# Optimization experiments

Measured on AMD Instinct MI355X. Metric: run time of the kernel, lower is better.

## Reference

```python
import jax, jax.numpy as jnp
import numpy as np

N = 50000      # nodes
E = 800000     # edges
D_IN, D_H, D_OUT = 256, 256, 128
BN_EPS = 1e-5


def setup_inputs() -> dict:
    key = jax.random.key(0)
    ks = jax.random.split(key, 16)
    inp = {}
    inp["x"] = jax.random.normal(ks[0], (N, D_IN), dtype=jnp.float32)
    inp["edge_index"] = jax.random.randint(ks[1], (2, E), 0, N, dtype=jnp.int32)
    s1 = 1.0 / np.sqrt(D_IN)
    s2 = 1.0 / np.sqrt(D_H)
    inp["W1"] = jax.random.normal(ks[2], (D_IN, D_H), dtype=jnp.float32) * s1
    inp["b1"] = jnp.zeros((D_H,), dtype=jnp.float32)
    inp["g1"] = jnp.ones((D_H,), dtype=jnp.float32)
    inp["be1"] = jnp.zeros((D_H,), dtype=jnp.float32)
    inp["m1"] = jax.random.normal(ks[3], (D_H,), dtype=jnp.float32) * 0.1
    inp["v1"] = jax.random.uniform(ks[4], (D_H,), dtype=jnp.float32, minval=0.5, maxval=1.5)
    inp["W2"] = jax.random.normal(ks[5], (D_H, D_H), dtype=jnp.float32) * s2
    inp["b2"] = jnp.zeros((D_H,), dtype=jnp.float32)
    inp["g2"] = jnp.ones((D_H,), dtype=jnp.float32)
    inp["be2"] = jnp.zeros((D_H,), dtype=jnp.float32)
    inp["m2"] = jax.random.normal(ks[6], (D_H,), dtype=jnp.float32) * 0.1
    inp["v2"] = jax.random.uniform(ks[7], (D_H,), dtype=jnp.float32, minval=0.5, maxval=1.5)
    inp["W3"] = jax.random.normal(ks[8], (D_H, D_OUT), dtype=jnp.float32) * s2
    inp["b3"] = jnp.zeros((D_OUT,), dtype=jnp.float32)
    return inp


def reference(x, edge_index, W1, b1, g1, be1, m1, v1,
              W2, b2, g2, be2, m2, v2, W3, b3):
    # Add self-loops (PyG GCNConv default) and compute symmetric normalization once.
    loop = jnp.arange(N, dtype=edge_index.dtype)
    src = jnp.concatenate([edge_index[0], loop])   # [E+N]
    dst = jnp.concatenate([edge_index[1], loop])   # [E+N]
    deg = jax.ops.segment_sum(jnp.ones_like(dst, dtype=x.dtype), dst, num_segments=N)
    dinv = jax.lax.rsqrt(deg)                      # deg >= 1 thanks to self-loops
    norm = (dinv[src] * dinv[dst])[:, None]        # [E+N, 1]

    def gcn_conv(h, W, b):
        h = h @ W                                   # [N, D]
        agg = jax.ops.segment_sum(h[src] * norm, dst, num_segments=N)
        return agg + b

    def bn_eval(h, g, be, m, v):
        return (h - m) * (g * jax.lax.rsqrt(v + BN_EPS)) + be

    h = jax.nn.relu(bn_eval(gcn_conv(x, W1, b1), g1, be1, m1, v1))  # dropout = identity (eval)
    h = jax.nn.relu(bn_eval(gcn_conv(h, W2, b2), g2, be2, m2, v2))
    out = gcn_conv(h, W3, b3)                       # [N, D_OUT]
    return out
```

## Files before the change

### kernel.cpp

```cpp
#include <hip/hip_runtime.h>
#include <hip/hip_bf16.h>
#include <hip/hip_fp16.h>


#define GN 50000
#define GE 800000

typedef float f32x4 __attribute__((ext_vector_type(4)));
typedef _Float16 f16x8 __attribute__((ext_vector_type(8)));


__global__ __launch_bounds__(256) void init_kernel(int* counts, int* cursor, int* total) {
    int i = blockIdx.x * 256 + threadIdx.x;
    if (i < GN) { counts[i] = 0; cursor[i] = 0; }
    if (i == 0) *total = 0;
}

__global__ __launch_bounds__(256) void count_kernel(const int* __restrict__ dst, int* __restrict__ counts) {
    int e = blockIdx.x * 256 + threadIdx.x;
    if (e < GE) atomicAdd(&counts[dst[e]], 1);
}

__global__ __launch_bounds__(256) void alloc_kernel(const int* __restrict__ counts, float* __restrict__ dinv,
                                                    int* __restrict__ base, int* __restrict__ total) {
    int i = blockIdx.x * 256 + threadIdx.x;
    int lane = threadIdx.x & 63;
    int c = (i < GN) ? counts[i] : 0;
    if (i < GN) dinv[i] = rsqrtf((float)c + 1.0f);
    int v = c;
#pragma unroll
    for (int off = 1; off < 64; off <<= 1) {
        int t = __shfl_up(v, off);
        if (lane >= off) v += t;
    }
    int waveSum = __shfl(v, 63);
    int wb = 0;
    if (lane == 63) wb = atomicAdd(total, waveSum);
    wb = __shfl(wb, 63);
    if (i < GN) base[i] = wb + v - c;
}

__global__ __launch_bounds__(256) void fill_kernel(const int* __restrict__ src, const int* __restrict__ dst,
                                                   const int* __restrict__ base, int* __restrict__ cursor,
                                                   int* __restrict__ col) {
    int e = blockIdx.x * 256 + threadIdx.x;
    if (e < GE) {
        int d = dst[e];
        int pos = base[d] + atomicAdd(&cursor[d], 1);
        col[pos] = src[e];
    }
}

__global__ __launch_bounds__(256) void params_kernel(
    const float* b1, const float* g1, const float* be1, const float* m1, const float* v1,
    const float* b2, const float* g2, const float* be2, const float* m2, const float* v2,
    float* prm) {
    int t = threadIdx.x;
    float s1 = g1[t] * rsqrtf(v1[t] + 1e-5f);
    prm[0 * 256 + t] = s1;
    prm[1 * 256 + t] = (b1[t] - m1[t]) * s1 + be1[t];
    float s2 = g2[t] * rsqrtf(v2[t] + 1e-5f);
    prm[2 * 256 + t] = s2;
    prm[3 * 256 + t] = (b2[t] - m2[t]) * s2 + be2[t];
}


__global__ __launch_bounds__(256) void conv_x(const float* __restrict__ in, ushort* __restrict__ out, int n4) {
    int i = blockIdx.x * 256 + threadIdx.x;
    if (i >= n4) return;
    float4 v = *(const float4*)&in[(size_t)i * 4];
    ushort4 h;
    h.x = __half_as_ushort(__float2half_rn(v.x));
    h.y = __half_as_ushort(__float2half_rn(v.y));
    h.z = __half_as_ushort(__float2half_rn(v.z));
    h.w = __half_as_ushort(__float2half_rn(v.w));
    *(ushort4*)&out[(size_t)i * 4] = h;
}

__global__ __launch_bounds__(256) void transpose_all(const float* __restrict__ W1, const float* __restrict__ W2,
                                                     const float* __restrict__ W3,
                                                     ushort* __restrict__ T1h, ushort* __restrict__ T1l,
                                                     ushort* __restrict__ T2h, ushort* __restrict__ T2l,
                                                     ushort* __restrict__ T3h, ushort* __restrict__ T3l) {
    int idx = blockIdx.x * 256 + threadIdx.x;
    const float* W;
    ushort *Th, *Tl;
    int i, DO;
    if (idx < 65536) { W = W1; Th = T1h; Tl = T1l; i = idx; DO = 256; }
    else if (idx < 131072) { W = W2; Th = T2h; Tl = T2l; i = idx - 65536; DO = 256; }
    else if (idx < 163840) { W = W3; Th = T3h; Tl = T3l; i = idx - 131072; DO = 128; }
    else return;
    int n = i >> 8, k = i & 255;
    float v = W[k * DO + n];
    __half h = __float2half_rn(v);
    Th[i] = __half_as_ushort(h);
    Tl[i] = __half_as_ushort(__float2half_rn(v - __half2float(h)));
}


template <int DO>
__global__ __launch_bounds__(256) void gemm_mfma(const ushort* __restrict__ A16, const ushort* __restrict__ Bhi,
                                                 const ushort* __restrict__ Blo, const float* __restrict__ dinv,
                                                 __half* __restrict__ C, int M) {
    __shared__ ushort lds[3][128][40];
    int tid = threadIdx.x;
    int lane = tid & 63;
    int wave = tid >> 6;
    int wm = wave >> 1, wn = wave & 1;
    int m0 = blockIdx.x * 128;
    int n0 = blockIdx.y * 128;
    int rsel = lane & 15;
    int ksel = (lane >> 4) * 8;

    f32x4 acc[4][4] = {};

    for (int k0 = 0; k0 < 256; k0 += 32) {
        auto stage = [&](const ushort* __restrict__ src, int baseRow, int rClamp, int p) {
#pragma unroll
            for (int j = 0; j < 2; j++) {
                int o = (tid + j * 256) * 16;
                int row = o >> 6;
                int kb = o & 63;
                int rg = min(baseRow + row, rClamp);
                uint4 v = *(const uint4*)((const char*)src + (size_t)rg * 512 + (size_t)k0 * 2 + kb);
                *(uint4*)((char*)&lds[p][row][0] + kb) = v;
            }
        };
        stage(A16, m0, M - 1, 0);
        stage(Bhi, n0, DO - 1, 1);
        stage(Blo, n0, DO - 1, 2);
        __syncthreads();

        f16x8 bh[4], bl[4];
#pragma unroll
        for (int ni = 0; ni < 4; ni++) {
            bh[ni] = *(const f16x8*)&lds[1][wn * 64 + ni * 16 + rsel][ksel];
            bl[ni] = *(const f16x8*)&lds[2][wn * 64 + ni * 16 + rsel][ksel];
        }
#pragma unroll
        for (int mi = 0; mi < 4; mi++) {
            f16x8 av = *(const f16x8*)&lds[0][wm * 64 + mi * 16 + rsel][ksel];
#pragma unroll
            for (int ni = 0; ni < 4; ni++) {
                acc[mi][ni] = __builtin_amdgcn_mfma_f32_16x16x32_f16(av, bh[ni], acc[mi][ni], 0, 0, 0);
                acc[mi][ni] = __builtin_amdgcn_mfma_f32_16x16x32_f16(av, bl[ni], acc[mi][ni], 0, 0, 0);
            }
        }
        __syncthreads();
    }

#pragma unroll
    for (int mi = 0; mi < 4; mi++) {
#pragma unroll
        for (int j = 0; j < 4; j++) {
            int r = m0 + wm * 64 + mi * 16 + (lane >> 4) * 4 + j;
            if (r < M) {
                float dv = dinv[r];
#pragma unroll
                for (int ni = 0; ni < 4; ni++) {
                    int c = n0 + wn * 64 + ni * 16 + rsel;
                    C[(size_t)r * DO + c] = __float2half_rn(acc[mi][ni][j] * dv);
                }
            }
        }
    }
}

template <int D, int MODE>
__global__ __launch_bounds__(256) void agg_kernel(const __half* __restrict__ Hs, const int* __restrict__ base,
                                                  const int* __restrict__ counts, const float* __restrict__ dinv,
                                                  const int* __restrict__ col,
                                                  const float* __restrict__ pa, const float* __restrict__ pc,
                                                  float* __restrict__ outF, ushort* __restrict__ outH, int M) {
    constexpr int V = D / 64;
    constexpr int P = V / 2;
    int w = blockIdx.x * 4 + (threadIdx.x >> 6);
    if (w >= M) return;
    int lane = threadIdx.x & 63;
    const char* gbase = (const char*)(Hs + lane * V);
    float2 acc2[P];
#pragma unroll
    for (int j = 0; j < P; j++) acc2[j] = make_float2(0.f, 0.f);

    auto accum32 = [&](unsigned bits, int j2) {
        __half2 h = *(__half2*)&bits;
        float2 f = __half22float2(h);
        acc2[j2].x += f.x;
        acc2[j2].y += f.y;
    };

    if constexpr (V == 4) {
        uint2 r = *(const uint2*)(gbase + (size_t)w * D * 2);
        accum32(r.x, 0); accum32(r.y, 1);
    } else {
        unsigned r = *(const unsigned*)(gbase + (size_t)w * D * 2);
        accum32(r, 0);
    }

    int e = base[w], end = e + counts[w];
    for (; e + 8 <= end; e += 8) {
        int idx[8];
#pragma unroll
        for (int t = 0; t < 8; t++) idx[t] = col[e + t];
        if constexpr (V == 4) {
            uint2 r[8];
#pragma unroll
            for (int t = 0; t < 8; t++) r[t] = *(const uint2*)(gbase + (size_t)idx[t] * (D * 2));
#pragma unroll
            for (int t = 0; t < 8; t++) { accum32(r[t].x, 0); accum32(r[t].y, 1); }
        } else {
            unsigned r[8];
#pragma unroll
            for (int t = 0; t < 8; t++) r[t] = *(const unsigned*)(gbase + (size_t)idx[t] * (D * 2));
#pragma unroll
            for (int t = 0; t < 8; t++) accum32(r[t], 0);
        }
    }
    for (; e < end; e++) {
        int s = col[e];
        if constexpr (V == 4) {
            uint2 r = *(const uint2*)(gbase + (size_t)s * (D * 2));
            accum32(r.x, 0); accum32(r.y, 1);
        } else {
            unsigned r = *(const unsigned*)(gbase + (size_t)s * (D * 2));
            accum32(r, 0);
        }
    }

    float dv = dinv[w];
    float acc[V];
#pragma unroll
    for (int j = 0; j < P; j++) { acc[2 * j] = acc2[j].x; acc[2 * j + 1] = acc2[j].y; }

    if constexpr (MODE == 1) {
        ushort4 h;
        int d = lane * V;
        float val;
        val = fmaxf(fmaf(acc[0] * dv, pa[d + 0], pc[d + 0]), 0.f);
        h.x = __half_as_ushort(__float2half_rn(val));
        val = fmaxf(fmaf(acc[1] * dv, pa[d + 1], pc[d + 1]), 0.f);
        h.y = __half_as_ushort(__float2half_rn(val));
        val = fmaxf(fmaf(acc[2] * dv, pa[d + 2], pc[d + 2]), 0.f);
        h.z = __half_as_ushort(__float2half_rn(val));
        val = fmaxf(fmaf(acc[3] * dv, pa[d + 3], pc[d + 3]), 0.f);
        h.w = __half_as_ushort(__float2half_rn(val));
        *(ushort4*)&outH[(size_t)w * D + d] = h;
    } else {
#pragma unroll
        for (int j = 0; j < V; j++) {
            int d = lane * V + j;
            outF[(size_t)w * D + d] = acc[j] * dv + pa[d];
        }
    }
}


extern "C" void kernel_launch(void* const* d_in, const int* in_sizes, int n_in,
                              void* d_out, int out_size, void* d_ws, size_t ws_size,
                              hipStream_t stream) {
    const float* x = (const float*)d_in[0];
    const int* ei = (const int*)d_in[1];
    const int* srcIdx = ei;
    const int* dstIdx = ei + GE;
    const float* W1 = (const float*)d_in[2];
    const float* b1 = (const float*)d_in[3];
    const float* g1 = (const float*)d_in[4];
    const float* be1 = (const float*)d_in[5];
    const float* m1 = (const float*)d_in[6];
    const float* v1 = (const float*)d_in[7];
    const float* W2 = (const float*)d_in[8];
    const float* b2 = (const float*)d_in[9];
    const float* g2 = (const float*)d_in[10];
    const float* be2 = (const float*)d_in[11];
    const float* m2 = (const float*)d_in[12];
    const float* v2 = (const float*)d_in[13];
    const float* W3 = (const float*)d_in[14];
    const float* b3 = (const float*)d_in[15];
    float* out = (float*)d_out;

    size_t off = 0;
    char* wsb = (char*)d_ws;
    auto take = [&](size_t bytes) -> char* {
        char* p = wsb + off;
        off += (bytes + 255) & ~(size_t)255;
        return p;
    };
    float* dinv = (float*)take((size_t)GN * 4);
    int* counts = (int*)take((size_t)GN * 4);
    int* cursor = (int*)take((size_t)GN * 4);
    int* segbase = (int*)take((size_t)GN * 4);
    int* total = (int*)take(256);
    int* col = (int*)take((size_t)GE * 4);
    float* prm = (float*)take(4 * 256 * 4);
    __half* hH = (__half*)take((size_t)GN * 256 * 2);
    ushort* P = (ushort*)take((size_t)GN * 256 * 2);
    ushort* X16 = P;
    ushort* WT1h = (ushort*)take(256 * 256 * 2);
    ushort* WT1l = (ushort*)take(256 * 256 * 2);
    ushort* WT2h = (ushort*)take(256 * 256 * 2);
    ushort* WT2l = (ushort*)take(256 * 256 * 2);
    ushort* WT3h = (ushort*)take(128 * 256 * 2);
    ushort* WT3l = (ushort*)take(128 * 256 * 2);

    const float* a1 = prm + 0 * 256;
    const float* c1 = prm + 1 * 256;
    const float* a2 = prm + 2 * 256;
    const float* c2 = prm + 3 * 256;

    int nb = (GN + 255) / 256;
    int eb = (GE + 255) / 256;

    init_kernel<<<nb, 256, 0, stream>>>(counts, cursor, total);
    count_kernel<<<eb, 256, 0, stream>>>(dstIdx, counts);
    alloc_kernel<<<nb, 256, 0, stream>>>(counts, dinv, segbase, total);
    fill_kernel<<<eb, 256, 0, stream>>>(srcIdx, dstIdx, segbase, cursor, col);
    params_kernel<<<1, 256, 0, stream>>>(b1, g1, be1, m1, v1, b2, g2, be2, m2, v2, prm);

    int n4 = GN * 64;
    conv_x<<<(n4 + 255) / 256, 256, 0, stream>>>(x, X16, n4);
    transpose_all<<<(163840 + 255) / 256, 256, 0, stream>>>(W1, W2, W3, WT1h, WT1l, WT2h, WT2l, WT3h, WT3l);

    dim3 gg((GN + 127) / 128, 2);
    dim3 gg3((GN + 127) / 128, 1);
    int ab = (GN + 3) / 4;

    gemm_mfma<256><<<gg, 256, 0, stream>>>(X16, WT1h, WT1l, dinv, hH, GN);
    agg_kernel<256, 1><<<ab, 256, 0, stream>>>(hH, segbase, counts, dinv, col, a1, c1, nullptr, P, GN);
    gemm_mfma<256><<<gg, 256, 0, stream>>>(P, WT2h, WT2l, dinv, hH, GN);
    agg_kernel<256, 1><<<ab, 256, 0, stream>>>(hH, segbase, counts, dinv, col, a2, c2, nullptr, P, GN);
    gemm_mfma<128><<<gg3, 256, 0, stream>>>(P, WT3h, WT3l, dinv, hH, GN);
    agg_kernel<128, 0><<<ab, 256, 0, stream>>>(hH, segbase, counts, dinv, col, b3, b3, out, nullptr, GN);
}
```

Before: 451.2 us.

## Prefetch next GEMM K-tile into registers and sort CSR neighbor lists

The MFMA GEMM now loads the next K-slice of A and the split-precision B tiles into registers while the current slice is computed from LDS, so global load latency overlaps with matrix math. A new kernel insertion-sorts each node's neighbor list after the atomic CSR fill, which makes gathers in aggregation more ordered and the float summation order deterministic. The sort adds a serial per-node pass with scattered global accesses. The register prefetch raises register pressure in the GEMM.

```diff
diff --git a/kernel.cpp b/kernel.cpp
--- a/kernel.cpp
+++ b/kernel.cpp
@@ -48,6 +48,19 @@
         int d = dst[e];
         int pos = base[d] + atomicAdd(&cursor[d], 1);
         col[pos] = src[e];
+    }
+}
+
+__global__ __launch_bounds__(256) void sort_kernel(const int* __restrict__ base, const int* __restrict__ counts,
+                                                   int* __restrict__ col) {
+    int w = blockIdx.x * 256 + threadIdx.x;
+    if (w >= GN) return;
+    int b = base[w], n = counts[w];
+    for (int i = 1; i < n; i++) {
+        int key = col[b + i];
+        int j = i - 1;
+        while (j >= 0 && col[b + j] > key) { col[b + j + 1] = col[b + j]; j--; }
+        col[b + j + 1] = key;
     }
 }
 
@@ -112,24 +125,40 @@
     int rsel = lane & 15;
     int ksel = (lane >> 4) * 8;
 
+    int o0 = tid * 16, o1 = (tid + 256) * 16;
+    int row0 = o0 >> 6, kb0 = o0 & 63;
+    int row1 = o1 >> 6, kb1 = o1 & 63;
+    int rA0 = min(m0 + row0, M - 1), rA1 = min(m0 + row1, M - 1);
+    int rB0 = min(n0 + row0, DO - 1), rB1 = min(n0 + row1, DO - 1);
+
+    uint4 vA0, vA1, vBh0, vBh1, vBl0, vBl1;
+    auto loadregs = [&](int k0) {
+        const char* a = (const char*)A16;
+        const char* bh = (const char*)Bhi;
+        const char* bl = (const char*)Blo;
+        vA0 = *(const uint4*)(a + (size_t)rA0 * 512 + (size_t)k0 * 2 + kb0);
+        vA1 = *(const uint4*)(a + (size_t)rA1 * 512 + (size_t)k0 * 2 + kb1);
+        vBh0 = *(const uint4*)(bh + (size_t)rB0 * 512 + (size_t)k0 * 2 + kb0);
+        vBh1 = *(const uint4*)(bh + (size_t)rB1 * 512 + (size_t)k0 * 2 + kb1);
+        vBl0 = *(const uint4*)(bl + (size_t)rB0 * 512 + (size_t)k0 * 2 + kb0);
+        vBl1 = *(const uint4*)(bl + (size_t)rB1 * 512 + (size_t)k0 * 2 + kb1);
+    };
+    auto writelds = [&]() {
+        *(uint4*)((char*)&lds[0][row0][0] + kb0) = vA0;
+        *(uint4*)((char*)&lds[0][row1][0] + kb1) = vA1;
+        *(uint4*)((char*)&lds[1][row0][0] + kb0) = vBh0;
+        *(uint4*)((char*)&lds[1][row1][0] + kb1) = vBh1;
+        *(uint4*)((char*)&lds[2][row0][0] + kb0) = vBl0;
+        *(uint4*)((char*)&lds[2][row1][0] + kb1) = vBl1;
+    };
+
     f32x4 acc[4][4] = {};
 
+    loadregs(0);
     for (int k0 = 0; k0 < 256; k0 += 32) {
-        auto stage = [&](const ushort* __restrict__ src, int baseRow, int rClamp, int p) {
-#pragma unroll
-            for (int j = 0; j < 2; j++) {
-                int o = (tid + j * 256) * 16;
-                int row = o >> 6;
-                int kb = o & 63;
-                int rg = min(baseRow + row, rClamp);
-                uint4 v = *(const uint4*)((const char*)src + (size_t)rg * 512 + (size_t)k0 * 2 + kb);
-                *(uint4*)((char*)&lds[p][row][0] + kb) = v;
-            }
-        };
-        stage(A16, m0, M - 1, 0);
-        stage(Bhi, n0, DO - 1, 1);
-        stage(Blo, n0, DO - 1, 2);
+        writelds();
         __syncthreads();
+        if (k0 + 32 < 256) loadregs(k0 + 32);
 
         f16x8 bh[4], bl[4];
 #pragma unroll
@@ -314,6 +343,7 @@
     count_kernel<<<eb, 256, 0, stream>>>(dstIdx, counts);
     alloc_kernel<<<nb, 256, 0, stream>>>(counts, dinv, segbase, total);
     fill_kernel<<<eb, 256, 0, stream>>>(srcIdx, dstIdx, segbase, cursor, col);
+    sort_kernel<<<nb, 256, 0, stream>>>(segbase, counts, col);
     params_kernel<<<1, 256, 0, stream>>>(b1, g1, be1, m1, v1, b2, g2, be2, m2, v2, prm);
 
     int n4 = GN * 64;
```

Result: slower. 537.5 us (+19.1%).
